# Performance work log

Measured on AMD Instinct MI355X. Metric: run time of the kernel, lower is better.

The kernel has to match this reference:

```python
import jax, jax.numpy as jnp
import numpy as np


def _mlp(x, w1, b1, w2, b2):
    # torch Mlp: fc1 -> GELU (exact erf) -> fc2, dropout off in eval
    h = jax.nn.gelu(x @ w1 + b1, approximate=False)
    return h @ w2 + b2


def _nearest(x, oh, ow):
    # torch F.interpolate mode='nearest' on [B,h,w,d]: src = floor(dst*in/out)
    h, w = x.shape[1], x.shape[2]
    ih = (np.arange(oh) * h) // oh
    iw = (np.arange(ow) * w) // ow
    return x[:, ih][:, :, iw]


def setup_inputs() -> dict:
    key = jax.random.key(0)
    ks = jax.random.split(key, 8)
    B, s0, dim, nPnt, new2 = 4, 12, 256, 128, 48  # new_size=24
    sc = 0.02
    return {
        "token_init": jax.random.normal(ks[0], (B, s0, s0, dim), jnp.float32),
        "point_token": jax.random.normal(ks[1], (B, nPnt, dim), jnp.float32),
        "nr_w1": jax.random.normal(ks[2], (nPnt, 4 * nPnt), jnp.float32) * sc,
        "nr_b1": jnp.zeros((4 * nPnt,), jnp.float32),
        "nr_w2": jax.random.normal(ks[3], (4 * nPnt, nPnt), jnp.float32) * sc,
        "nr_b2": jnp.zeros((nPnt,), jnp.float32),
        "na_w1": jax.random.normal(ks[4], (nPnt, 4 * nPnt), jnp.float32) * sc,
        "na_b1": jnp.zeros((4 * nPnt,), jnp.float32),
        "na_w2": jax.random.normal(ks[5], (4 * nPnt, nPnt), jnp.float32) * sc,
        "na_b2": jnp.zeros((nPnt,), jnp.float32),
        "tf_w1": jax.random.normal(ks[6], (new2, new2), jnp.float32) * sc,
        "tf_b1": jnp.zeros((new2,), jnp.float32),
        "tf_w2": jax.random.normal(ks[7], (new2, 1), jnp.float32) * sc,
        "tf_b2": jnp.zeros((1,), jnp.float32),
        "height": 120,
        "width": 160,
    }


def reference(token_init, point_token, nr_w1, nr_b1, nr_w2, nr_b2,
              na_w1, na_b1, na_w2, na_b2, tf_w1, tf_b1, tf_w2, tf_b2,
              height, width):
    B, nPnt, dim = point_token.shape
    new_size = tf_w1.shape[0] // 2
    scale = dim ** (-0.5)
    # is_init=False path: repeat_interleave x2 along H and W
    t = jnp.repeat(jnp.repeat(token_init, 2, axis=1), 2, axis=2)  # [B,2s,2s,d]
    token_raw = _nearest(t, height, width)                        # [B,H,W,d]
    t_exp = _nearest(t, new_size, new_size)                       # [B,sH,sW,d]
    sH = sW = new_size
    token_templ = t_exp.reshape(B, sH * sW, dim)
    node_adj = jnp.einsum('bnd,bpd->bnp', token_templ, point_token) * scale
    node_adj = _mlp(node_adj, nr_w1, nr_b1, nr_w2, nr_b2)
    node_adj = node_adj.reshape(B, sH, sW, nPnt)
    node_w = jnp.einsum('bhwp,bhwd->bhpd', node_adj, t_exp) * (sW ** -0.5)
    node_h = jnp.einsum('bhwp,bhwd->bwpd', node_adj, t_exp) * (sH ** -0.5)
    token_n = jnp.concatenate([node_w, node_h], axis=1)           # [B,2s,nPnt,d]
    x = token_n.reshape(B, sH + sW, nPnt * dim).transpose(0, 2, 1)  # [B,nPnt*d,2s]
    token_fused = _mlp(x, tf_w1, tf_b1, tf_w2, tf_b2)             # [B,nPnt*d,1]
    token_fused = token_fused.reshape(B, nPnt, dim)
    token_raw_f = token_raw.reshape(B, height * width, dim)
    node_attn = jnp.einsum('bnd,bpd->bnp', token_raw_f, point_token) * scale
    node_attn = jax.nn.softmax(_mlp(node_attn, na_w1, na_b1, na_w2, na_b2), axis=-1)
    token_new = node_attn @ token_fused + token_raw_f             # [B,HW,d]
    return token_new
```

## Files before the change

kernel.cpp:

```cpp
#include <hip/hip_runtime.h>
#include <math.h>

#define B     4
#define DIM   256
#define NP    128
#define NS    144
#define HID   512
#define NROW  576
#define H_OUT 120
#define W_OUT 160

__device__ __forceinline__ float gelu_exact(float x) {
    return 0.5f * x * (1.0f + erff(x * 0.70710678118654752440f));
}

__global__ __launch_bounds__(256) void k_t(
    const float* __restrict__ pt, const float* __restrict__ tf_w1,
    float* __restrict__ ptT, float* __restrict__ w1pg)
{
    const int bid = blockIdx.x;
    const int t   = threadIdx.x;

    if (bid == 128) {
        for (int i = t; i < 24 * 48; i += 256) {
            const int m = i / 48, k = i - m * 48;
            w1pg[i] = tf_w1[(2 * m) * 48 + k] + tf_w1[(2 * m + 1) * 48 + k];
        }
        return;
    }

    const int b   = bid >> 5;
    const int rem = bid & 31;
    const int d0  = (rem >> 2) * 32;
    const int p0  = (rem & 3) * 32;
    __shared__ float tile[32][33];

    #pragma unroll
    for (int i = t; i < 1024; i += 256) {
        const int row = i >> 5, col = i & 31;
        tile[row][col] = pt[(size_t)(b * NP + p0 + row) * DIM + d0 + col];
    }
    __syncthreads();
    #pragma unroll
    for (int i = t; i < 1024; i += 256) {
        const int row = i >> 5, col = i & 31;
        ptT[(size_t)(b * DIM + d0 + row) * NP + p0 + col] = tile[col][row];
    }
}

__global__ __launch_bounds__(256) void k_mlp(
    const float* __restrict__ ti, const float* __restrict__ ptT,
    const float* __restrict__ nr_w1, const float* __restrict__ nr_b1,
    const float* __restrict__ nr_w2, const float* __restrict__ nr_b2,
    const float* __restrict__ na_w1, const float* __restrict__ na_b1,
    const float* __restrict__ na_w2, const float* __restrict__ na_b2,
    float* __restrict__ nadjT, float* __restrict__ attn)
{
    const int mlp  = blockIdx.x / 144;
    const int tile = blockIdx.x % 144;
    const int g0 = tile * 4;
    const int b  = g0 / NS;
    const int n0 = g0 % NS;
    const int t  = threadIdx.x;

    const float* __restrict__ w1 = mlp ? na_w1 : nr_w1;
    const float* __restrict__ b1 = mlp ? na_b1 : nr_b1;
    const float* __restrict__ w2 = mlp ? na_w2 : nr_w2;
    const float* __restrict__ b2 = mlp ? na_b2 : nr_b2;

    __shared__ float xs[4][DIM];
    __shared__ float parA[8][4][NP];
    __shared__ float qs[4][NP];
    __shared__ float hs[4][HID];
    __shared__ float par[8][4][NP];
    __shared__ float wred[4][2];

    {
        const int r = t >> 6, c = t & 63;
        ((float4*)xs[r])[c] = ((const float4*)ti)[(size_t)(g0 + r) * 64 + c];
    }
    __syncthreads();

    {
        const int pq = t & 31;
        const int dg = t >> 5;
        const float4* __restrict__ pT4 =
            (const float4*)(ptT + (size_t)b * DIM * NP) + pq;
        float4 a0 = make_float4(0.f,0.f,0.f,0.f);
        float4 a1 = a0, a2 = a0, a3 = a0;
        #pragma unroll 8
        for (int d2 = 0; d2 < 32; ++d2) {
            const int d = dg * 32 + d2;
            const float4 v4 = pT4[(size_t)d * 32];
            const float x0 = xs[0][d], x1 = xs[1][d];
            const float x2 = xs[2][d], x3 = xs[3][d];
            a0.x += x0*v4.x; a0.y += x0*v4.y; a0.z += x0*v4.z; a0.w += x0*v4.w;
            a1.x += x1*v4.x; a1.y += x1*v4.y; a1.z += x1*v4.z; a1.w += x1*v4.w;
            a2.x += x2*v4.x; a2.y += x2*v4.y; a2.z += x2*v4.z; a2.w += x2*v4.w;
            a3.x += x3*v4.x; a3.y += x3*v4.y; a3.z += x3*v4.z; a3.w += x3*v4.w;
        }
        ((float4*)parA[dg][0])[pq] = a0;
        ((float4*)parA[dg][1])[pq] = a1;
        ((float4*)parA[dg][2])[pq] = a2;
        ((float4*)parA[dg][3])[pq] = a3;
    }
    __syncthreads();

    const int p  = t & 127;
    const int rh = t >> 7;
    {
        float q0 = 0.f, q1 = 0.f;
        #pragma unroll
        for (int dg = 0; dg < 8; ++dg) {
            q0 += parA[dg][rh][p];
            q1 += parA[dg][rh + 2][p];
        }
        qs[rh][p]     = q0 * 0.0625f;
        qs[rh + 2][p] = q1 * 0.0625f;
    }
    __syncthreads();

    {
        const int kq = t & 127;
        const int k0 = kq * 4;
        float4 acc0 = *(const float4*)(b1 + k0);
        float4 acc1 = acc0;
        const float* __restrict__ wp = w1 + k0;
        #pragma unroll 16
        for (int pp = 0; pp < NP; ++pp) {
            const float4 w4 = *(const float4*)(wp + (size_t)pp * HID);
            const float q0 = qs[rh][pp];
            const float q1 = qs[rh + 2][pp];
            acc0.x += q0*w4.x; acc0.y += q0*w4.y;
            acc0.z += q0*w4.z; acc0.w += q0*w4.w;
            acc1.x += q1*w4.x; acc1.y += q1*w4.y;
            acc1.z += q1*w4.z; acc1.w += q1*w4.w;
        }
        float4 o0, o1;
        o0.x = gelu_exact(acc0.x); o0.y = gelu_exact(acc0.y);
        o0.z = gelu_exact(acc0.z); o0.w = gelu_exact(acc0.w);
        o1.x = gelu_exact(acc1.x); o1.y = gelu_exact(acc1.y);
        o1.z = gelu_exact(acc1.z); o1.w = gelu_exact(acc1.w);
        ((float4*)hs[rh])[kq]     = o0;
        ((float4*)hs[rh + 2])[kq] = o1;
    }
    __syncthreads();

    {
        const int pq = t & 31;
        const int p0 = pq * 4;
        const int kg = t >> 5;
        float4 a0 = make_float4(0.f,0.f,0.f,0.f);
        float4 a1 = a0, a2 = a0, a3 = a0;
        const float4* __restrict__ w24 = (const float4*)(w2 + p0);
        #pragma unroll 8
        for (int i = 0; i < 64; ++i) {
            const int k = kg * 64 + i;
            const float4 w4 = w24[(size_t)k * 32];
            const float h0 = hs[0][k], h1 = hs[1][k];
            const float h2 = hs[2][k], h3 = hs[3][k];
            a0.x += h0*w4.x; a0.y += h0*w4.y; a0.z += h0*w4.z; a0.w += h0*w4.w;
            a1.x += h1*w4.x; a1.y += h1*w4.y; a1.z += h1*w4.z; a1.w += h1*w4.w;
            a2.x += h2*w4.x; a2.y += h2*w4.y; a2.z += h2*w4.z; a2.w += h2*w4.w;
            a3.x += h3*w4.x; a3.y += h3*w4.y; a3.z += h3*w4.z; a3.w += h3*w4.w;
        }
        ((float4*)par[kg][0])[pq] = a0;
        ((float4*)par[kg][1])[pq] = a1;
        ((float4*)par[kg][2])[pq] = a2;
        ((float4*)par[kg][3])[pq] = a3;
    }
    __syncthreads();

    float lg0 = b2[p], lg1 = lg0;
    #pragma unroll
    for (int kg = 0; kg < 8; ++kg) {
        lg0 += par[kg][rh][p];
        lg1 += par[kg][rh + 2][p];
    }

    if (mlp == 0) {
        float* __restrict__ dst = nadjT + (size_t)(b * NP + p) * NS + n0;
        dst[rh]     = lg0;
        dst[rh + 2] = lg1;
    } else {
        const int wid   = t >> 6;
        const int wpair = wid ^ 1;
        float m0 = lg0, m1 = lg1;
        #pragma unroll
        for (int off = 32; off > 0; off >>= 1) {
            m0 = fmaxf(m0, __shfl_xor(m0, off));
            m1 = fmaxf(m1, __shfl_xor(m1, off));
        }
        if ((t & 63) == 0) { wred[wid][0] = m0; wred[wid][1] = m1; }
        __syncthreads();
        m0 = fmaxf(m0, wred[wpair][0]);
        m1 = fmaxf(m1, wred[wpair][1]);

        const float e0 = expf(lg0 - m0), e1 = expf(lg1 - m1);
        float s0 = e0, s1 = e1;
        #pragma unroll
        for (int off = 32; off > 0; off >>= 1) {
            s0 += __shfl_xor(s0, off);
            s1 += __shfl_xor(s1, off);
        }
        __syncthreads();
        if ((t & 63) == 0) { wred[wid][0] = s0; wred[wid][1] = s1; }
        __syncthreads();
        s0 += wred[wpair][0];
        s1 += wred[wpair][1];

        attn[(size_t)(g0 + rh) * NP + p]     = e0 / s0;
        attn[(size_t)(g0 + rh + 2) * NP + p] = e1 / s1;
    }
}

__global__ __launch_bounds__(256) void k_fold(
    const float* __restrict__ nadjT, const float* __restrict__ ti,
    const float* __restrict__ w1p,
    const float* __restrict__ b1, const float* __restrict__ w2,
    const float* __restrict__ b2, float* __restrict__ tf)
{
    const int b = blockIdx.x >> 7;
    const int p = blockIdx.x & 127;
    const int t = threadIdx.x;

    const float* __restrict__ an = nadjT + (size_t)(b * NP + p) * NS;
    const int d = t;
    const float* __restrict__ tb = ti + (size_t)b * NS * DIM + d;

    float v[24];
    #pragma unroll
    for (int m = 0; m < 24; ++m) v[m] = 0.f;
    #pragma unroll
    for (int y = 0; y < 12; ++y) {
        #pragma unroll
        for (int x = 0; x < 12; ++x) {
            const int n = y * 12 + x;
            const float tv = tb[n * DIM];
            const float a  = an[n];
            v[y]      += a * tv;
            v[12 + x] += a * tv;
        }
    }
    const float c = 0.40824829046386301637f;
    #pragma unroll
    for (int m = 0; m < 24; ++m) v[m] *= c;

    float acc = b2[0];
    for (int k = 0; k < 48; ++k) {
        float tt = b1[k];
        #pragma unroll
        for (int m = 0; m < 24; ++m) tt += v[m] * w1p[m * 48 + k];
        acc += gelu_exact(tt) * w2[k];
    }
    tf[(size_t)(b * NP + p) * DIM + d] = acc;
}

__global__ __launch_bounds__(256) void k_final(
    const float* __restrict__ attn, const float* __restrict__ tf,
    const float* __restrict__ ti, float4* __restrict__ out)
{
    const int g = blockIdx.x;
    const int b = g / NS;
    const int n = g % NS;
    const int t = threadIdx.x;
    const int dq = t & 63;
    const int pg = t >> 6;

    __shared__ float  at[NP];
    __shared__ float4 par4[4][64];
    __shared__ float4 rowf[64];

    if (t < NP) at[t] = attn[(size_t)g * NP + t];
    __syncthreads();

    const float4* __restrict__ tp = (const float4*)tf + (size_t)b * NP * 64 + dq;
    float4 acc = make_float4(0.f, 0.f, 0.f, 0.f);
    #pragma unroll 16
    for (int i = 0; i < 32; ++i) {
        const int pp = pg * 32 + i;
        const float  a  = at[pp];
        const float4 tv = tp[(size_t)pp * 64];
        acc.x += a * tv.x; acc.y += a * tv.y;
        acc.z += a * tv.z; acc.w += a * tv.w;
    }
    par4[pg][dq] = acc;
    __syncthreads();

    if (t < 64) {
        float4 s = par4[0][t];
        const float4 s1 = par4[1][t], s2 = par4[2][t], s3 = par4[3][t];
        const float4 tiv = ((const float4*)ti)[(size_t)g * 64 + t];
        s.x += s1.x + s2.x + s3.x + tiv.x;
        s.y += s1.y + s2.y + s3.y + tiv.y;
        s.z += s1.z + s2.z + s3.z + tiv.z;
        s.w += s1.w + s2.w + s3.w + tiv.w;
        rowf[t] = s;
    }
    __syncthreads();

    const int y = n / 12, x = n % 12;
    const int w_lo = (40 * x + 2) / 3;
    const int w_hi = (40 * x + 42) / 3;
    const float4 val = rowf[dq];
    const int h0 = 10 * y;
    for (int h = h0; h < h0 + 10; ++h) {
        float4* __restrict__ orow = out + (size_t)((b * H_OUT + h) * W_OUT) * 64 + dq;
        for (int w = w_lo + pg; w < w_hi; w += 4) {
            orow[(size_t)w * 64] = val;
        }
    }
}

extern "C" void kernel_launch(void* const* d_in, const int* in_sizes, int n_in,
                              void* d_out, int out_size, void* d_ws, size_t ws_size,
                              hipStream_t stream) {
    (void)in_sizes; (void)n_in; (void)out_size; (void)ws_size;
    const float* token_init  = (const float*)d_in[0];
    const float* point_token = (const float*)d_in[1];
    const float* nr_w1 = (const float*)d_in[2];
    const float* nr_b1 = (const float*)d_in[3];
    const float* nr_w2 = (const float*)d_in[4];
    const float* nr_b2 = (const float*)d_in[5];
    const float* na_w1 = (const float*)d_in[6];
    const float* na_b1 = (const float*)d_in[7];
    const float* na_w2 = (const float*)d_in[8];
    const float* na_b2 = (const float*)d_in[9];
    const float* tf_w1 = (const float*)d_in[10];
    const float* tf_b1 = (const float*)d_in[11];
    const float* tf_w2 = (const float*)d_in[12];
    const float* tf_b2 = (const float*)d_in[13];

    float* out = (float*)d_out;
    float* ws  = (float*)d_ws;
    float* nadjT = ws;
    float* attn  = nadjT + NROW * NP;
    float* tf    = attn + NROW * NP;
    float* ptT   = tf + B * NP * DIM;
    float* w1pg  = ptT + B * DIM * NP;

    k_t<<<129, 256, 0, stream>>>(point_token, tf_w1, ptT, w1pg);
    k_mlp<<<288, 256, 0, stream>>>(token_init, ptT,
                                   nr_w1, nr_b1, nr_w2, nr_b2,
                                   na_w1, na_b1, na_w2, na_b2,
                                   nadjT, attn);
    k_fold<<<B * NP, 256, 0, stream>>>(nadjT, token_init, w1pg,
                                       tf_b1, tf_w2, tf_b2, tf);
    k_final<<<NROW, 256, 0, stream>>>(attn, tf, token_init, (float4*)out);
}
```

Measured before the change: 160.7 us.

## Drop transpose kernel, read point tokens directly, use fast GELU approximation

Removes the separate transpose kernel by having k_mlp read point_token rows directly. Each thread pair reduces one point's dot products with a shuffle, and the tf_w1 pair-sum moves into an extra block of k_mlp. The first MLP layer is reorganised so each thread computes 2 hidden units for all 4 rows, reading q values from a transposed shared array. Exact erf GELU is replaced by an exp2/rcp sigmoid-style approximation in both MLP kernels, which trades a small amount of accuracy for fewer instructions. The goal is to cut a kernel launch, the ptT workspace round trip, one sync stage and the transcendental cost.

New measurement: 161.9 us. Within noise of the previous version (+0.8%).

```diff
diff --git a/kernel.cpp b/kernel.cpp
--- a/kernel.cpp
+++ b/kernel.cpp
@@ -10,58 +10,39 @@
 #define H_OUT 120
 #define W_OUT 160
 
-__device__ __forceinline__ float gelu_exact(float x) {
-    return 0.5f * x * (1.0f + erff(x * 0.70710678118654752440f));
-}
-
-__global__ __launch_bounds__(256) void k_t(
-    const float* __restrict__ pt, const float* __restrict__ tf_w1,
-    float* __restrict__ ptT, float* __restrict__ w1pg)
-{
-    const int bid = blockIdx.x;
-    const int t   = threadIdx.x;
-
-    if (bid == 128) {
-        for (int i = t; i < 24 * 48; i += 256) {
-            const int m = i / 48, k = i - m * 48;
-            w1pg[i] = tf_w1[(2 * m) * 48 + k] + tf_w1[(2 * m + 1) * 48 + k];
-        }
-        return;
-    }
-
-    const int b   = bid >> 5;
-    const int rem = bid & 31;
-    const int d0  = (rem >> 2) * 32;
-    const int p0  = (rem & 3) * 32;
-    __shared__ float tile[32][33];
-
-    #pragma unroll
-    for (int i = t; i < 1024; i += 256) {
-        const int row = i >> 5, col = i & 31;
-        tile[row][col] = pt[(size_t)(b * NP + p0 + row) * DIM + d0 + col];
-    }
-    __syncthreads();
-    #pragma unroll
-    for (int i = t; i < 1024; i += 256) {
-        const int row = i >> 5, col = i & 31;
-        ptT[(size_t)(b * DIM + d0 + row) * NP + p0 + col] = tile[col][row];
-    }
+__device__ __forceinline__ float gelu_fast(float x) {
+    const float x2 = x * x;
+    const float u  = x * (2.302052793f + 0.10293626f * x2);
+    const float e  = exp2f(u);
+    const float r  = __builtin_amdgcn_rcpf(e + 1.0f);
+    return x - x * r;
 }
 
 __global__ __launch_bounds__(256) void k_mlp(
-    const float* __restrict__ ti, const float* __restrict__ ptT,
+    const float* __restrict__ ti, const float* __restrict__ pt,
     const float* __restrict__ nr_w1, const float* __restrict__ nr_b1,
     const float* __restrict__ nr_w2, const float* __restrict__ nr_b2,
     const float* __restrict__ na_w1, const float* __restrict__ na_b1,
     const float* __restrict__ na_w2, const float* __restrict__ na_b2,
-    float* __restrict__ nadjT, float* __restrict__ attn)
+    const float* __restrict__ tf_w1,
+    float* __restrict__ nadjT, float* __restrict__ attn,
+    float* __restrict__ w1pg)
 {
+    const int t = threadIdx.x;
+
+    if (blockIdx.x == 288) {
+        for (int i = t; i < 24 * 48; i += 256) {
+            const int m = i / 48, k = i - m * 48;
+            w1pg[i] = tf_w1[(2 * m) * 48 + k] + tf_w1[(2 * m + 1) * 48 + k];
+        }
+        return;
+    }
+
     const int mlp  = blockIdx.x / 144;
     const int tile = blockIdx.x % 144;
     const int g0 = tile * 4;
     const int b  = g0 / NS;
     const int n0 = g0 % NS;
-    const int t  = threadIdx.x;
 
     const float* __restrict__ w1 = mlp ? na_w1 : nr_w1;
     const float* __restrict__ b1 = mlp ? na_b1 : nr_b1;
@@ -69,8 +50,7 @@
     const float* __restrict__ b2 = mlp ? na_b2 : nr_b2;
 
     __shared__ float xs[4][DIM];
-    __shared__ float parA[8][4][NP];
-    __shared__ float qs[4][NP];
+    __shared__ float qsT[NP][4];
     __shared__ float hs[4][HID];
     __shared__ float par[8][4][NP];
     __shared__ float wred[4][2];
@@ -82,67 +62,66 @@
     __syncthreads();
 
     {
-        const int pq = t & 31;
-        const int dg = t >> 5;
-        const float4* __restrict__ pT4 =
-            (const float4*)(ptT + (size_t)b * DIM * NP) + pq;
+        const int p  = t >> 1;
+        const int dh = t & 1;
+        const float4* __restrict__ pt4 =
+            (const float4*)(pt + (size_t)(b * NP + p) * DIM) + dh * 32;
+        const float4* __restrict__ x0p = (const float4*)xs[0] + dh * 32;
+        const float4* __restrict__ x1p = (const float4*)xs[1] + dh * 32;
+        const float4* __restrict__ x2p = (const float4*)xs[2] + dh * 32;
+        const float4* __restrict__ x3p = (const float4*)xs[3] + dh * 32;
         float4 a0 = make_float4(0.f,0.f,0.f,0.f);
         float4 a1 = a0, a2 = a0, a3 = a0;
         #pragma unroll 8
-        for (int d2 = 0; d2 < 32; ++d2) {
-            const int d = dg * 32 + d2;
-            const float4 v4 = pT4[(size_t)d * 32];
-            const float x0 = xs[0][d], x1 = xs[1][d];
-            const float x2 = xs[2][d], x3 = xs[3][d];
-            a0.x += x0*v4.x; a0.y += x0*v4.y; a0.z += x0*v4.z; a0.w += x0*v4.w;
-            a1.x += x1*v4.x; a1.y += x1*v4.y; a1.z += x1*v4.z; a1.w += x1*v4.w;
-            a2.x += x2*v4.x; a2.y += x2*v4.y; a2.z += x2*v4.z; a2.w += x2*v4.w;
-            a3.x += x3*v4.x; a3.y += x3*v4.y; a3.z += x3*v4.z; a3.w += x3*v4.w;
-        }
-        ((float4*)parA[dg][0])[pq] = a0;
-        ((float4*)parA[dg][1])[pq] = a1;
-        ((float4*)parA[dg][2])[pq] = a2;
-        ((float4*)parA[dg][3])[pq] = a3;
-    }
-    __syncthreads();
-
-    const int p  = t & 127;
-    const int rh = t >> 7;
+        for (int i = 0; i < 32; ++i) {
+            const float4 pv = pt4[i];
+            const float4 x0 = x0p[i], x1 = x1p[i];
+            const float4 x2 = x2p[i], x3 = x3p[i];
+            a0.x += x0.x*pv.x; a0.y += x0.y*pv.y; a0.z += x0.z*pv.z; a0.w += x0.w*pv.w;
+            a1.x += x1.x*pv.x; a1.y += x1.y*pv.y; a1.z += x1.z*pv.z; a1.w += x1.w*pv.w;
+            a2.x += x2.x*pv.x; a2.y += x2.y*pv.y; a2.z += x2.z*pv.z; a2.w += x2.w*pv.w;
+            a3.x += x3.x*pv.x; a3.y += x3.y*pv.y; a3.z += x3.z*pv.z; a3.w += x3.w*pv.w;
+        }
+        float s0 = (a0.x + a0.y) + (a0.z + a0.w);
+        float s1 = (a1.x + a1.y) + (a1.z + a1.w);
+        float s2 = (a2.x + a2.y) + (a2.z + a2.w);
+        float s3 = (a3.x + a3.y) + (a3.z + a3.w);
+        s0 += __shfl_xor(s0, 1);
+        s1 += __shfl_xor(s1, 1);
+        s2 += __shfl_xor(s2, 1);
+        s3 += __shfl_xor(s3, 1);
+        if (dh == 0) {
+            qsT[p][0] = s0 * 0.0625f;
+            qsT[p][1] = s1 * 0.0625f;
+            qsT[p][2] = s2 * 0.0625f;
+            qsT[p][3] = s3 * 0.0625f;
+        }
+    }
+    __syncthreads();
+
     {
-        float q0 = 0.f, q1 = 0.f;
-        #pragma unroll
-        for (int dg = 0; dg < 8; ++dg) {
-            q0 += parA[dg][rh][p];
-            q1 += parA[dg][rh + 2][p];
-        }
-        qs[rh][p]     = q0 * 0.0625f;
-        qs[rh + 2][p] = q1 * 0.0625f;
-    }
-    __syncthreads();
-
-    {
-        const int kq = t & 127;
-        const int k0 = kq * 4;
-        float4 acc0 = *(const float4*)(b1 + k0);
-        float4 acc1 = acc0;
+        const int k0 = 2 * t;
+        const float2 bv = *(const float2*)(b1 + k0);
+        float2 a0 = bv, a1 = bv, a2 = bv, a3 = bv;
         const float* __restrict__ wp = w1 + k0;
         #pragma unroll 16
         for (int pp = 0; pp < NP; ++pp) {
-            const float4 w4 = *(const float4*)(wp + (size_t)pp * HID);
-            const float q0 = qs[rh][pp];
-            const float q1 = qs[rh + 2][pp];
-            acc0.x += q0*w4.x; acc0.y += q0*w4.y;
-            acc0.z += q0*w4.z; acc0.w += q0*w4.w;
-            acc1.x += q1*w4.x; acc1.y += q1*w4.y;
-            acc1.z += q1*w4.z; acc1.w += q1*w4.w;
-        }
-        float4 o0, o1;
-        o0.x = gelu_exact(acc0.x); o0.y = gelu_exact(acc0.y);
-        o0.z = gelu_exact(acc0.z); o0.w = gelu_exact(acc0.w);
-        o1.x = gelu_exact(acc1.x); o1.y = gelu_exact(acc1.y);
-        o1.z = gelu_exact(acc1.z); o1.w = gelu_exact(acc1.w);
-        ((float4*)hs[rh])[kq]     = o0;
-        ((float4*)hs[rh + 2])[kq] = o1;
+            const float2 wv = *(const float2*)(wp + (size_t)pp * HID);
+            const float4 q  = *(const float4*)qsT[pp];
+            a0.x += q.x*wv.x; a0.y += q.x*wv.y;
+            a1.x += q.y*wv.x; a1.y += q.y*wv.y;
+            a2.x += q.z*wv.x; a2.y += q.z*wv.y;
+            a3.x += q.w*wv.x; a3.y += q.w*wv.y;
+        }
+        float2 o;
+        o.x = gelu_fast(a0.x); o.y = gelu_fast(a0.y);
+        *(float2*)(&hs[0][k0]) = o;
+        o.x = gelu_fast(a1.x); o.y = gelu_fast(a1.y);
+        *(float2*)(&hs[1][k0]) = o;
+        o.x = gelu_fast(a2.x); o.y = gelu_fast(a2.y);
+        *(float2*)(&hs[2][k0]) = o;
+        o.x = gelu_fast(a3.x); o.y = gelu_fast(a3.y);
+        *(float2*)(&hs[3][k0]) = o;
     }
     __syncthreads();
 
@@ -171,6 +150,8 @@
     }
     __syncthreads();
 
+    const int p  = t & 127;
+    const int rh = t >> 7;
     float lg0 = b2[p], lg1 = lg0;
     #pragma unroll
     for (int kg = 0; kg < 8; ++kg) {
@@ -251,7 +232,7 @@
         float tt = b1[k];
         #pragma unroll
         for (int m = 0; m < 24; ++m) tt += v[m] * w1p[m * 48 + k];
-        acc += gelu_exact(tt) * w2[k];
+        acc += gelu_fast(tt) * w2[k];
     }
     tf[(size_t)(b * NP + p) * DIM + d] = acc;
 }
@@ -336,14 +317,12 @@
     float* nadjT = ws;
     float* attn  = nadjT + NROW * NP;
     float* tf    = attn + NROW * NP;
-    float* ptT   = tf + B * NP * DIM;
-    float* w1pg  = ptT + B * DIM * NP;
-
-    k_t<<<129, 256, 0, stream>>>(point_token, tf_w1, ptT, w1pg);
-    k_mlp<<<288, 256, 0, stream>>>(token_init, ptT,
+    float* w1pg  = tf + B * NP * DIM;
+
+    k_mlp<<<289, 256, 0, stream>>>(token_init, point_token,
                                    nr_w1, nr_b1, nr_w2, nr_b2,
                                    na_w1, na_b1, na_w2, na_b2,
-                                   nadjT, attn);
+                                   tf_w1, nadjT, attn, w1pg);
     k_fold<<<B * NP, 256, 0, stream>>>(nadjT, token_init, w1pg,
                                        tf_b1, tf_w2, tf_b2, tf);
     k_final<<<NROW, 256, 0, stream>>>(attn, tf, token_init, (float4*)out);
```
